# Performance work log

Measured on AMD Instinct MI355X. Metric: run time of the kernel, lower is better.

The kernel has to match this reference:

```python
import jax, jax.numpy as jnp
import numpy as np

B, S, D, H = 4, 2048, 512, 8
HD = D // H  # head dim = 64
NEG = 1e9


def setup_inputs() -> dict:
    key = jax.random.key(0)
    ks = jax.random.split(key, 10)
    x = jax.random.normal(ks[0], (B, S, D), dtype=jnp.float32)
    group_ids = jnp.sort(jax.random.randint(ks[1], (B, S), 0, 8), axis=-1)
    s = 0.05
    Wq = jax.random.normal(ks[2], (D, D), dtype=jnp.float32) * s
    Wk = jax.random.normal(ks[3], (D, D), dtype=jnp.float32) * s
    Wv = jax.random.normal(ks[4], (D, D), dtype=jnp.float32) * s
    Wo = jax.random.normal(ks[5], (D, D), dtype=jnp.float32) * s
    bq = jnp.zeros((D,), jnp.float32)
    bk = jnp.zeros((D,), jnp.float32)
    bv = jnp.zeros((D,), jnp.float32)
    bo = jnp.zeros((D,), jnp.float32)
    return {"x": x, "group_ids": group_ids, "Wq": Wq, "bq": bq,
            "Wk": Wk, "bk": bk, "Wv": Wv, "bv": bv, "Wo": Wo, "bo": bo}


def reference(x, group_ids, Wq, bq, Wk, bk, Wv, bv, Wo, bo):
    relu = jax.nn.relu
    # projections + activation (activation='relu' is applied to q,k,v AND output)
    q = relu(x @ Wq + bq)  # [B,S,D]
    k = relu(x @ Wk + bk)
    v = relu(x @ Wv + bv)
    # split heads -> [B,H,S,HD]
    def split(t):
        return t.reshape(B, S, H, HD).transpose(0, 2, 1, 3)
    qh, kh, vh = split(q), split(k), split(v)
    # note: scale uses feature dim AFTER head split, i.e. head_dim
    scale = 1.0 / jnp.sqrt(jnp.float32(HD))
    e = jnp.einsum('bhqd,bhkd->bhqk', qh, kh) * scale  # [B,H,S,S]
    group_mask = (group_ids[:, None, :, None] == group_ids[:, None, None, :])  # [B,1,S,S]
    e = e - (1.0 - group_mask.astype(jnp.float32)) * NEG
    a = jax.nn.softmax(e, axis=-1)
    yh = jnp.einsum('bhqk,bhkd->bhqd', a, vh)  # [B,H,S,HD]
    y = yh.transpose(0, 2, 1, 3).reshape(B, S, D)
    return relu(y @ Wo + bo)
```

## Files before the change

kernel.cpp:

```cpp
#include <hip/hip_runtime.h>
#include <cmath>

#define Bsz 4
#define Ssz 2048
#define Dsz 512
#define Hn 8

typedef unsigned short u16;
typedef _Float16 f16;
typedef __attribute__((ext_vector_type(4))) _Float16 f16x4;
typedef __attribute__((ext_vector_type(8))) _Float16 f16x8;
typedef __attribute__((ext_vector_type(8))) unsigned short us8;
typedef __attribute__((ext_vector_type(4))) float f32x4;
typedef __attribute__((ext_vector_type(16))) float f32x16;

__device__ __forceinline__ void gl2lds16(const void* g, void* l) {
    __builtin_amdgcn_global_load_lds(
        (const __attribute__((address_space(1))) void*)g,
        (__attribute__((address_space(3))) void*)l, 16, 0, 0);
}

__global__ __launch_bounds__(256) void prep(const float* __restrict__ x,
                                            f16* __restrict__ xb,
                                            const float* __restrict__ Wq,
                                            const float* __restrict__ Wk,
                                            const float* __restrict__ Wv,
                                            const float* __restrict__ Wo,
                                            f16* __restrict__ Wtqkv,
                                            f16* __restrict__ Wto) {
    const int blk = blockIdx.x;
    const int tid = threadIdx.x;
    if (blk < 2048) {
        int i = blk * 256 + tid;
        const float4* xv = (const float4*)x;
        float4 a = xv[2 * i], b = xv[2 * i + 1];
        f16x8 o;
        o[0] = (f16)a.x; o[1] = (f16)a.y; o[2] = (f16)a.z; o[3] = (f16)a.w;
        o[4] = (f16)b.x; o[5] = (f16)b.y; o[6] = (f16)b.z; o[7] = (f16)b.w;
        ((f16x8*)xb)[i] = o;
        return;
    }
    __shared__ float T[64][65];
    const int bz = blk - 2048;
    const int z = bz >> 6;
    const int n0 = (bz & 7) * 64, k0 = ((bz >> 3) & 7) * 64;
    const float* W = (z == 0) ? Wq : (z == 1) ? Wk : (z == 2) ? Wv : Wo;
    const float sc = (z == 0) ? 0.125f : 1.0f;
#pragma unroll
    for (int i = 0; i < 16; i++) {
        int e = tid + i * 256;
        int r = e >> 6, c = e & 63;
        T[r][c] = W[(size_t)(k0 + r) * Dsz + n0 + c];
    }
    __syncthreads();
    f16* dst = (z < 3) ? (Wtqkv + ((size_t)z * 512 + n0) * Dsz + k0)
                       : (Wto + (size_t)n0 * Dsz + k0);
#pragma unroll
    for (int i = 0; i < 16; i++) {
        int e = tid + i * 256;
        int r = e >> 6, c = e & 63;
        dst[(size_t)r * Dsz + c] = (f16)(T[c][r] * sc);
    }
}

template <int MODE>
__global__ __launch_bounds__(256) void gemm128(
    const f16* __restrict__ A, const f16* __restrict__ Bt,
    u16* o0, u16* o1, u16* o2v,
    const float* b0, const float* b1, const float* b2,
    float* ofp, const float* bias_f) {
    __shared__ __align__(16) u16 smem[2 * 128 * 64];
    u16* As = smem;
    u16* Bs = smem + 128 * 64;
    const int tid = threadIdx.x;
    const int colg0 = blockIdx.x * 128;
    const int row0 = blockIdx.y * 128;
    const int w = tid >> 6, lane = tid & 63;
    const int nn = lane & 31, hh = lane >> 5;
    const int wr = w >> 1, wc = w & 1;

    f32x16 acc[2][2];
#pragma unroll
    for (int bi = 0; bi < 2; bi++)
#pragma unroll
        for (int bj = 0; bj < 2; bj++)
#pragma unroll
            for (int e = 0; e < 16; e++) acc[bi][bj][e] = 0.f;

    const f16* Ablk = A + (size_t)row0 * 512;
    const f16* Bblk = Bt + (size_t)colg0 * 512;

    for (int k0 = 0; k0 < 512; k0 += 64) {
        __syncthreads();
#pragma unroll
        for (int i = 0; i < 4; i++) {
            int p = tid + i * 256;
            int m = p >> 3, kc = p & 7;
            int gk = ((kc ^ (m & 7)) << 3);
            gl2lds16(Ablk + (size_t)m * 512 + k0 + gk, As + p * 8);
            gl2lds16(Bblk + (size_t)m * 512 + k0 + gk, Bs + p * 8);
        }
        __syncthreads();
#pragma unroll
        for (int t = 0; t < 4; t++) {
            f16x8 af[2], bfr[2];
#pragma unroll
            for (int bi = 0; bi < 2; bi++) {
                int r = wr * 64 + bi * 32 + nn;
                int ch = r * 8 + ((t * 2 + hh) ^ (r & 7));
                af[bi] = *(const f16x8*)(As + ch * 8);
            }
#pragma unroll
            for (int bj = 0; bj < 2; bj++) {
                int n = wc * 64 + bj * 32 + nn;
                int ch = n * 8 + ((t * 2 + hh) ^ (n & 7));
                bfr[bj] = *(const f16x8*)(Bs + ch * 8);
            }
#pragma unroll
            for (int bi = 0; bi < 2; bi++)
#pragma unroll
                for (int bj = 0; bj < 2; bj++)
                    acc[bi][bj] = __builtin_amdgcn_mfma_f32_32x32x16_f16(
                        af[bi], bfr[bj], acc[bi][bj], 0, 0, 0);
        }
    }

    if (MODE == 0) {
        const int sel = colg0 >> 9;
        const int c0 = colg0 & 511;
        if (sel < 2) {
            u16* outp = (sel == 0) ? o0 : o1;
            const float* bp = (sel == 0) ? b0 : b1;
            const float bscale = (sel == 0) ? 0.125f : 1.0f;
#pragma unroll
            for (int bj = 0; bj < 2; bj++) {
                int col = c0 + wc * 64 + bj * 32 + nn;
                float bv = bp[col] * bscale;
                int head = col >> 6, dd = col & 63;
#pragma unroll
                for (int bi = 0; bi < 2; bi++)
#pragma unroll
                    for (int rg = 0; rg < 16; rg++) {
                        int row = row0 + wr * 64 + bi * 32 +
                                  (rg & 3) + 8 * (rg >> 2) + 4 * hh;
                        f16 v = (f16)fmaxf(acc[bi][bj][rg] + bv, 0.f);
                        size_t dst;
                        if (sel == 0) {
                            dst = (size_t)row * 512 + col;
                        } else {
                            int bb = row >> 11, ss = row & 2047;
                            int tt = ss >> 6, ii = ss & 63;
                            dst = (((size_t)((bb * 8 + head) * 32 + tt)) << 12)
                                  + ii * 64 + dd;
                        }
                        *(f16*)(outp + dst) = v;
                    }
            }
        } else {
            const int hh_head = c0 >> 6;
            f16 (*T)[136] = (f16(*)[136])smem;
            const int bb = row0 >> 11;
            const int t0 = (row0 & 2047) >> 6;
            __syncthreads();
#pragma unroll
            for (int ph = 0; ph < 2; ph++) {
                if (wc == ph) {
#pragma unroll
                    for (int bj = 0; bj < 2; bj++) {
                        int d = bj * 32 + nn;
                        float bv = b2[c0 + ph * 64 + d];
#pragma unroll
                        for (int bi = 0; bi < 2; bi++)
#pragma unroll
                            for (int rg = 0; rg < 16; rg++) {
                                int s = wr * 64 + bi * 32 +
                                        (rg & 3) + 8 * (rg >> 2) + 4 * hh;
                                T[d][s] = (f16)fmaxf(acc[bi][bj][rg] + bv, 0.f);
                            }
                    }
                }
                __syncthreads();
#pragma unroll
                for (int ii = 0; ii < 4; ii++) {
                    int oct = tid + ii * 256;
                    int tt = oct >> 9, rem = oct & 511;
                    int d = rem >> 3, s8 = rem & 7;
                    us8 val = *(const us8*)(&T[d][tt * 64 + s8 * 8]);
                    size_t dst = (((size_t)((bb * 8 + hh_head + ph) * 32 + t0 + tt)) << 12)
                                 + d * 64 + s8 * 8;
                    *(us8*)(o2v + dst) = val;
                }
                __syncthreads();
            }
        }
    } else {
#pragma unroll
        for (int bj = 0; bj < 2; bj++) {
            int col = colg0 + wc * 64 + bj * 32 + nn;
            float bv = bias_f[col];
#pragma unroll
            for (int bi = 0; bi < 2; bi++)
#pragma unroll
                for (int rg = 0; rg < 16; rg++) {
                    int row = row0 + wr * 64 + bi * 32 +
                              (rg & 3) + 8 * (rg >> 2) + 4 * hh;
                    ofp[(size_t)row * 512 + col] = fmaxf(acc[bi][bj][rg] + bv, 0.f);
                }
        }
    }
}

__global__ __launch_bounds__(512) void attn_mfma(
    const f16* __restrict__ Q, const u16* __restrict__ KP,
    const u16* __restrict__ VT, const int* __restrict__ G,
    f16* __restrict__ Y) {
    __shared__ __align__(16) u16 Ks[2][4096];
    __shared__ __align__(16) u16 Vs[2][4096];

    const int qt = blockIdx.x, h = blockIdx.y, b = blockIdx.z;
    const int q0 = qt * 128;
    const int tid = threadIdx.x;
    const int w = tid >> 6, lane = tid & 63;
    const int ln = lane & 15, quad = lane >> 4;

    const f16* Qb = Q + (size_t)b * Ssz * Dsz;
    const u16* Ktb = KP + (size_t)(b * Hn + h) * 32 * 4096;
    const u16* Vtb = VT + (size_t)(b * Hn + h) * 32 * 4096;
    const int* Gb = G + (size_t)b * Ssz;

    f16x8 qf[2];
    {
        const f16* qrow = Qb + (size_t)(q0 + w * 16 + ln) * Dsz + h * 64;
        qf[0] = *(const f16x8*)(qrow + quad * 8);
        qf[1] = *(const f16x8*)(qrow + 32 + quad * 8);
    }
    const int gq = Gb[q0 + w * 16 + ln];
    const int gqmin = Gb[q0], gqmax = Gb[q0 + 127];

    int gf = 0, gl = 0; bool ov = false;
    if (lane < 32) {
        gf = Gb[lane * 64]; gl = Gb[lane * 64 + 63];
        ov = (gl >= gqmin) && (gf <= gqmax);
    }
    unsigned long long mask = __ballot(ov);
    const int kt_lo = __builtin_ctzll(mask);
    const int kt_hi = 63 - __builtin_clzll(mask);

    f32x4 o[4];
    const f32x4 z4 = {0.f, 0.f, 0.f, 0.f};
#pragma unroll
    for (int nd = 0; nd < 4; nd++) o[nd] = z4;
    float lsum = 0.f;

#define STAGE_T(base, kt, dstbuf)                                              \
    {                                                                          \
        const u16* tile = (base) + (size_t)(kt) * 4096;                        \
        int row = tid >> 3, c = tid & 7;                                       \
        gl2lds16(tile + row * 64 + ((c ^ (row & 7)) << 3),                     \
                 (dstbuf) + tid * 8);                                          \
    }

    STAGE_T(Ktb, kt_lo, Ks[0])
    STAGE_T(Vtb, kt_lo, Vs[0])

    int buf = 0;
    for (int kt = kt_lo; kt <= kt_hi; kt++) {
        __syncthreads();
        if (kt < kt_hi) {
            STAGE_T(Ktb, kt + 1, Ks[buf ^ 1])
            STAGE_T(Vtb, kt + 1, Vs[buf ^ 1])
        }
        const u16* ks = Ks[buf];
        const u16* vs = Vs[buf];
        const int k0 = kt * 64;
        const int gkf = __shfl(gf, kt), gkl = __shfl(gl, kt);
        const bool needMask = !(gqmin == gqmax && gkf == gkl);

        f16x4 pf[4];
#pragma unroll
        for (int kb = 0; kb < 4; kb++) {
            f32x4 s = z4;
#pragma unroll
            for (int kk = 0; kk < 2; kk++) {
                int key = kb * 16 + ln;
                int ch = key * 8 + ((kk * 4 + quad) ^ (key & 7));
                f16x8 kf = *(const f16x8*)(ks + ch * 8);
                s = __builtin_amdgcn_mfma_f32_16x16x32_f16(kf, qf[kk], s, 0, 0, 0);
            }
            float sv[4];
            if (needMask) {
                int4 g4 = *(const int4*)(Gb + k0 + kb * 16 + quad * 4);
                sv[0] = (gq == g4.x) ? s[0] - 4.0f : -1e9f;
                sv[1] = (gq == g4.y) ? s[1] - 4.0f : -1e9f;
                sv[2] = (gq == g4.z) ? s[2] - 4.0f : -1e9f;
                sv[3] = (gq == g4.w) ? s[3] - 4.0f : -1e9f;
            } else {
#pragma unroll
                for (int r = 0; r < 4; r++) sv[r] = s[r] - 4.0f;
            }
            f16x4 pp;
#pragma unroll
            for (int r = 0; r < 4; r++) {
                float e = __expf(sv[r]);
                lsum += e;
                pp[r] = (f16)e;
            }
            pf[kb] = pp;
        }
#pragma unroll
        for (int nd = 0; nd < 4; nd++)
#pragma unroll
            for (int kc = 0; kc < 4; kc++) {
                int addr = (((nd * 16 + ln) * 8 +
                             ((kc * 2 + (quad >> 1)) ^ (ln & 7))) << 3) +
                           (quad & 1) * 4;
                f16x4 vf = *(const f16x4*)(vs + addr);
                o[nd] = __builtin_amdgcn_mfma_f32_16x16x16f16(pf[kc], vf, o[nd], 0, 0, 0);
            }
        buf ^= 1;
    }

    lsum += __shfl_xor(lsum, 16);
    lsum += __shfl_xor(lsum, 32);
    float linv = 1.0f / lsum;
#pragma unroll
    for (int r = 0; r < 4; r++) {
        float lr = __shfl(linv, (lane & 48) | (quad * 4 + r));
        size_t row = (size_t)b * Ssz + q0 + w * 16 + quad * 4 + r;
#pragma unroll
        for (int nd = 0; nd < 4; nd++)
            Y[row * Dsz + h * 64 + nd * 16 + ln] = (f16)(o[nd][r] * lr);
    }
#undef STAGE_T
}

extern "C" void kernel_launch(void* const* d_in, const int* in_sizes, int n_in,
                              void* d_out, int out_size, void* d_ws, size_t ws_size,
                              hipStream_t stream) {
    const float* x  = (const float*)d_in[0];
    const int*   g  = (const int*)d_in[1];
    const float* Wq = (const float*)d_in[2];
    const float* bq = (const float*)d_in[3];
    const float* Wk = (const float*)d_in[4];
    const float* bk = (const float*)d_in[5];
    const float* Wv = (const float*)d_in[6];
    const float* bv = (const float*)d_in[7];
    const float* Wo = (const float*)d_in[8];
    const float* bo = (const float*)d_in[9];
    float* out = (float*)d_out;

    const size_t E = (size_t)Bsz * Ssz * Dsz;
    f16* xb  = (f16*)d_ws;
    f16* qb  = xb + E;
    u16* kpb = (u16*)(qb + E);
    u16* vtb = kpb + E;
    f16* yb  = (f16*)(vtb + E);
    f16* Wtqkv = yb + E;
    f16* Wto   = Wtqkv + 1536 * 512;

    prep<<<2304, 256, 0, stream>>>(x, xb, Wq, Wk, Wv, Wo, Wtqkv, Wto);
    gemm128<0><<<dim3(12, 64), 256, 0, stream>>>(xb, Wtqkv, (u16*)qb, kpb, vtb,
                                                 bq, bk, bv, nullptr, nullptr);
    attn_mfma<<<dim3(Ssz / 128, Hn, Bsz), 512, 0, stream>>>(qb, kpb, vtb, g, yb);
    gemm128<1><<<dim3(4, 64), 256, 0, stream>>>(yb, Wto, nullptr, nullptr, nullptr,
                                                nullptr, nullptr, nullptr,
                                                out, bo);
}
```

Before: 153.2 us.

## Double-buffer GEMM LDS loads and use exp2 with log2e-folded Q scale

The projection GEMM now stages K in 32-wide chunks into two LDS buffers, issuing the next chunk's global-to-LDS loads before computing on the current one, so loads overlap MFMA work. It also uses a new swizzled layout for the half-width tiles. The attention softmax switches from __expf to exp2f, with log2(e) folded into the Q weight and bias scale and the fixed max-offset constant adjusted to match. This removes a multiply per exponential but relies on the fixed offset staying numerically safe in base 2.

```diff
diff --git a/kernel.cpp b/kernel.cpp
--- a/kernel.cpp
+++ b/kernel.cpp
@@ -45,7 +45,7 @@
     const int z = bz >> 6;
     const int n0 = (bz & 7) * 64, k0 = ((bz >> 3) & 7) * 64;
     const float* W = (z == 0) ? Wq : (z == 1) ? Wk : (z == 2) ? Wv : Wo;
-    const float sc = (z == 0) ? 0.125f : 1.0f;
+    const float sc = (z == 0) ? 0.18033688f : 1.0f;
 #pragma unroll
     for (int i = 0; i < 16; i++) {
         int e = tid + i * 256;
@@ -69,9 +69,7 @@
     u16* o0, u16* o1, u16* o2v,
     const float* b0, const float* b1, const float* b2,
     float* ofp, const float* bias_f) {
-    __shared__ __align__(16) u16 smem[2 * 128 * 64];
-    u16* As = smem;
-    u16* Bs = smem + 128 * 64;
+    __shared__ __align__(16) u16 smem[4 * 4096];
     const int tid = threadIdx.x;
     const int colg0 = blockIdx.x * 128;
     const int row0 = blockIdx.y * 128;
@@ -90,40 +88,54 @@
     const f16* Ablk = A + (size_t)row0 * 512;
     const f16* Bblk = Bt + (size_t)colg0 * 512;
 
+#define GSTAGE(k0_, ab)                                                        \
+    {                                                                          \
+        _Pragma("unroll") for (int i = 0; i < 2; i++) {                        \
+            int p = tid + i * 256;                                             \
+            int L = p >> 3, c8 = (p & 7) ^ (L & 7);                            \
+            int m = 2 * L + (c8 >> 2), kc = c8 & 3;                            \
+            gl2lds16(Ablk + (size_t)m * 512 + (k0_) + kc * 8,                  \
+                     smem + (ab) * 4096 + p * 8);                              \
+            gl2lds16(Bblk + (size_t)m * 512 + (k0_) + kc * 8,                  \
+                     smem + 8192 + (ab) * 4096 + p * 8);                       \
+        }                                                                      \
+    }
+
+#define FRAG(bufbase, r, kc)                                                   \
+    (*(const f16x8*)(smem + (bufbase) +                                        \
+                     (((r) >> 1) * 8 + ((((r) & 1) * 4 + (kc)) ^ (((r) >> 1) & 7))) * 8))
+
+#define GCOMPUTE(ab)                                                           \
+    {                                                                          \
+        _Pragma("unroll") for (int t = 0; t < 2; t++) {                        \
+            f16x8 af[2], bfr[2];                                               \
+            _Pragma("unroll") for (int bi = 0; bi < 2; bi++) {                 \
+                int r = wr * 64 + bi * 32 + nn;                                \
+                af[bi] = FRAG((ab) * 4096, r, t * 2 + hh);                     \
+            }                                                                  \
+            _Pragma("unroll") for (int bj = 0; bj < 2; bj++) {                 \
+                int n = wc * 64 + bj * 32 + nn;                                \
+                bfr[bj] = FRAG(8192 + (ab) * 4096, n, t * 2 + hh);             \
+            }                                                                  \
+            _Pragma("unroll") for (int bi = 0; bi < 2; bi++)                   \
+                _Pragma("unroll") for (int bj = 0; bj < 2; bj++)               \
+                    acc[bi][bj] = __builtin_amdgcn_mfma_f32_32x32x16_f16(      \
+                        af[bi], bfr[bj], acc[bi][bj], 0, 0, 0);                \
+        }                                                                      \
+    }
+
+    GSTAGE(0, 0)
     for (int k0 = 0; k0 < 512; k0 += 64) {
         __syncthreads();
-#pragma unroll
-        for (int i = 0; i < 4; i++) {
-            int p = tid + i * 256;
-            int m = p >> 3, kc = p & 7;
-            int gk = ((kc ^ (m & 7)) << 3);
-            gl2lds16(Ablk + (size_t)m * 512 + k0 + gk, As + p * 8);
-            gl2lds16(Bblk + (size_t)m * 512 + k0 + gk, Bs + p * 8);
-        }
+        GSTAGE(k0 + 32, 1)
+        GCOMPUTE(0)
         __syncthreads();
-#pragma unroll
-        for (int t = 0; t < 4; t++) {
-            f16x8 af[2], bfr[2];
-#pragma unroll
-            for (int bi = 0; bi < 2; bi++) {
-                int r = wr * 64 + bi * 32 + nn;
-                int ch = r * 8 + ((t * 2 + hh) ^ (r & 7));
-                af[bi] = *(const f16x8*)(As + ch * 8);
-            }
-#pragma unroll
-            for (int bj = 0; bj < 2; bj++) {
-                int n = wc * 64 + bj * 32 + nn;
-                int ch = n * 8 + ((t * 2 + hh) ^ (n & 7));
-                bfr[bj] = *(const f16x8*)(Bs + ch * 8);
-            }
-#pragma unroll
-            for (int bi = 0; bi < 2; bi++)
-#pragma unroll
-                for (int bj = 0; bj < 2; bj++)
-                    acc[bi][bj] = __builtin_amdgcn_mfma_f32_32x32x16_f16(
-                        af[bi], bfr[bj], acc[bi][bj], 0, 0, 0);
-        }
-    }
+        if (k0 + 64 < 512) GSTAGE(k0 + 64, 0)
+        GCOMPUTE(1)
+    }
+#undef GSTAGE
+#undef FRAG
+#undef GCOMPUTE
 
     if (MODE == 0) {
         const int sel = colg0 >> 9;
@@ -131,7 +143,7 @@
         if (sel < 2) {
             u16* outp = (sel == 0) ? o0 : o1;
             const float* bp = (sel == 0) ? b0 : b1;
-            const float bscale = (sel == 0) ? 0.125f : 1.0f;
+            const float bscale = (sel == 0) ? 0.18033688f : 1.0f;
 #pragma unroll
             for (int bj = 0; bj < 2; bj++) {
                 int col = c0 + wc * 64 + bj * 32 + nn;
@@ -290,18 +302,18 @@
             float sv[4];
             if (needMask) {
                 int4 g4 = *(const int4*)(Gb + k0 + kb * 16 + quad * 4);
-                sv[0] = (gq == g4.x) ? s[0] - 4.0f : -1e9f;
-                sv[1] = (gq == g4.y) ? s[1] - 4.0f : -1e9f;
-                sv[2] = (gq == g4.z) ? s[2] - 4.0f : -1e9f;
-                sv[3] = (gq == g4.w) ? s[3] - 4.0f : -1e9f;
+                sv[0] = (gq == g4.x) ? s[0] - 5.7708f : -1e9f;
+                sv[1] = (gq == g4.y) ? s[1] - 5.7708f : -1e9f;
+                sv[2] = (gq == g4.z) ? s[2] - 5.7708f : -1e9f;
+                sv[3] = (gq == g4.w) ? s[3] - 5.7708f : -1e9f;
             } else {
 #pragma unroll
-                for (int r = 0; r < 4; r++) sv[r] = s[r] - 4.0f;
+                for (int r = 0; r < 4; r++) sv[r] = s[r] - 5.7708f;
             }
             f16x4 pp;
 #pragma unroll
             for (int r = 0; r < 4; r++) {
-                float e = __expf(sv[r]);
+                float e = exp2f(sv[r]);
                 lsum += e;
                 pp[r] = (f16)e;
             }
```

New measurement: 154.6 us. About the same (+1.0%).
